# Performance work log

Measured on AMD Instinct MI355X. Metric: run time of the kernel, lower is better.

Reference implementation:

```python
import jax, jax.numpy as jnp
import numpy as np

NUM_CLASSES = 100000
FEAT_DIM = 128
BATCH = 16384
LOSS_WEIGHT = 0.01


def setup_inputs() -> dict:
    key = jax.random.key(0)
    k1, k2, k3 = jax.random.split(key, 3)
    y = jax.random.randint(k1, (BATCH,), 0, NUM_CLASSES, dtype=jnp.int64)
    feat = jax.random.normal(k2, (BATCH, FEAT_DIM), dtype=jnp.float32)
    centers = jax.random.normal(k3, (NUM_CLASSES, FEAT_DIM), dtype=jnp.float32)
    return {"y": y, "feat": feat, "centers": centers}


def reference(y, feat, centers):
    # hist: per-class counts (torch.histc with unit-width bins over [0, num_classes])
    counts = jax.ops.segment_sum(jnp.ones((feat.shape[0],), feat.dtype), y,
                                 num_segments=NUM_CLASSES)  # [C]
    # per-class mean of features; zeros for empty classes (sum is 0 there)
    feat_sum = jax.ops.segment_sum(feat, y, num_segments=NUM_CLASSES)  # [C, D]
    feat_mean = feat_sum / jnp.maximum(counts, 1.0)[:, None]
    ratio = counts / (1.0 + counts)  # hist / (1 + hist)
    centers_grad = ratio[:, None] * (centers - feat_mean)  # [C, D]
    diff = feat - centers[y]  # gather centers per sample
    loss = LOSS_WEIGHT * 0.5 * jnp.sum(diff * diff)
    return (loss, centers_grad)
```

## Files before the change

### kernel.cpp

```cpp
#include <hip/hip_runtime.h>


#define BATCH   16384
#define FEAT    128
#define NCLASS  100000
#define LOSS_W  0.01f
#define CAP     32
#define NPART   12500

typedef float v4f __attribute__((ext_vector_type(4)));

__global__ __launch_bounds__(256)
void k_hist(const int* __restrict__ y,
            int* __restrict__ cnt,
            int* __restrict__ bucket) {
    int i = blockIdx.x * 256 + threadIdx.x;
    int c = y[i];
    int r = atomicAdd(cnt + c, 1);
    if (r < CAP) bucket[c * CAP + r] = i;
}

__global__ __launch_bounds__(256)
void k_grad_loss(const float* __restrict__ centers,
                 const int* __restrict__ cnt,
                 const int* __restrict__ bucket,
                 const float* __restrict__ feat,
                 float* __restrict__ grad,
                 float* __restrict__ partial) {
    int wid  = (blockIdx.x * 256 + threadIdx.x) >> 6;
    int lane = threadIdx.x & 63;
    int c    = wid * 2 + (lane >> 5);
    int q    = lane & 31;
    int n = cnt[c];

    v4f ce = (v4f)(0.0f);
    if (n > 0)
        ce = __builtin_nontemporal_load(
                 (const v4f*)(centers + (size_t)c * FEAT) + q);

    int m = n < CAP ? n : CAP;
    v4f acc = (v4f)(0.0f);
    float ls = 0.0f;
    for (int k = 0; k < m; k++) {
        int i = bucket[c * CAP + k];
        v4f f = __builtin_nontemporal_load(
                    (const v4f*)(feat + (size_t)i * FEAT) + q);
        acc += f;
        v4f d = f - ce;
        ls += d.x*d.x + d.y*d.y + d.z*d.z + d.w*d.w;
    }

    v4f o = (v4f)(0.0f);
    if (n > 0) {
        float inv   = 1.0f / (float)n;
        float ratio = (float)n / (1.0f + (float)n);
        o = ratio * (ce - acc * inv);
    }
    __builtin_nontemporal_store(o, (v4f*)(grad + (size_t)c * FEAT) + q);

    #pragma unroll
    for (int off = 32; off > 0; off >>= 1)
        ls += __shfl_down(ls, off, 64);
    __shared__ float smem[4];
    if (lane == 0) smem[threadIdx.x >> 6] = ls;
    __syncthreads();
    if (threadIdx.x == 0)
        partial[blockIdx.x] = smem[0] + smem[1] + smem[2] + smem[3];
}

__global__ __launch_bounds__(256)
void k_loss_final(const float* __restrict__ partial,
                  float* __restrict__ loss) {
    float s = 0.0f;
    const v4f* p4 = (const v4f*)partial;
    for (int i = threadIdx.x; i < NPART / 4; i += 256) {
        v4f v = p4[i];
        s += v.x + v.y + v.z + v.w;
    }
    #pragma unroll
    for (int off = 32; off > 0; off >>= 1)
        s += __shfl_down(s, off, 64);
    __shared__ float smem[4];
    if ((threadIdx.x & 63) == 0) smem[threadIdx.x >> 6] = s;
    __syncthreads();
    if (threadIdx.x == 0)
        *loss = LOSS_W * 0.5f * (smem[0] + smem[1] + smem[2] + smem[3]);
}

extern "C" void kernel_launch(void* const* d_in, const int* in_sizes, int n_in,
                              void* d_out, int out_size, void* d_ws, size_t ws_size,
                              hipStream_t stream) {
    const int*   y       = (const int*)d_in[0];
    const float* feat    = (const float*)d_in[1];
    const float* centers = (const float*)d_in[2];

    float* loss = (float*)d_out;
    float* grad = (float*)d_out + 1;

    int*   cnt     = (int*)d_ws;
    int*   bucket  = cnt + NCLASS;
    float* partial = (float*)(bucket + (size_t)NCLASS * CAP);

    (void)hipMemsetAsync(cnt, 0, (size_t)NCLASS * sizeof(int), stream);

    k_hist<<<BATCH / 256, 256, 0, stream>>>(y, cnt, bucket);

    k_grad_loss<<<NPART, 256, 0, stream>>>(
        centers, cnt, bucket, feat, grad, partial);

    k_loss_final<<<1, 256, 0, stream>>>(partial, loss);
}
```

Before: 125.5 us.

## Move loss into histogram kernel and fold final reduction into grad launch

The squared-error loss is now computed per sample in the histogram kernel, which gathers centers by label, instead of per class inside the gradient kernel. The gradient kernel gets one extra block that reduces the 1024 partial sums into the loss, which removes the separate single-block final reduction launch. This cuts one kernel launch and the serial tail reduction over 12500 partials, and slims the gradient loop. In exchange, feat is read twice and centers gathered an extra time, adding memory traffic. The loss now also counts samples beyond the per-class bucket cap.

```diff
diff --git a/kernel.cpp b/kernel.cpp
--- a/kernel.cpp
+++ b/kernel.cpp
@@ -6,27 +6,71 @@
 #define NCLASS  100000
 #define LOSS_W  0.01f
 #define CAP     32
-#define NPART   12500
+#define NGRAD   12500
+#define K1_BLK  1024
 
 typedef float v4f __attribute__((ext_vector_type(4)));
 
 __global__ __launch_bounds__(256)
-void k_hist(const int* __restrict__ y,
-            int* __restrict__ cnt,
-            int* __restrict__ bucket) {
-    int i = blockIdx.x * 256 + threadIdx.x;
-    int c = y[i];
-    int r = atomicAdd(cnt + c, 1);
-    if (r < CAP) bucket[c * CAP + r] = i;
+void k_hist_loss(const int* __restrict__ y,
+                 const float* __restrict__ feat,
+                 const float* __restrict__ centers,
+                 int* __restrict__ cnt,
+                 int* __restrict__ bucket,
+                 float* __restrict__ partial) {
+    int tid = blockIdx.x * 256 + threadIdx.x;
+
+    if (tid < BATCH) {
+        int c = y[tid];
+        int r = atomicAdd(cnt + c, 1);
+        if (r < CAP) bucket[c * CAP + r] = tid;
+    }
+
+    int hw = tid >> 5;
+    int q  = tid & 31;
+    float ls = 0.0f;
+    #pragma unroll
+    for (int s = 0; s < 2; s++) {
+        int i = hw * 2 + s;
+        int c = y[i];
+        v4f f  = *((const v4f*)(feat    + (size_t)i * FEAT) + q);
+        v4f ce = *((const v4f*)(centers + (size_t)c * FEAT) + q);
+        v4f d = f - ce;
+        ls += d.x*d.x + d.y*d.y + d.z*d.z + d.w*d.w;
+    }
+
+    #pragma unroll
+    for (int off = 32; off > 0; off >>= 1)
+        ls += __shfl_down(ls, off, 64);
+    __shared__ float smem[4];
+    if ((threadIdx.x & 63) == 0) smem[threadIdx.x >> 6] = ls;
+    __syncthreads();
+    if (threadIdx.x == 0)
+        partial[blockIdx.x] = smem[0] + smem[1] + smem[2] + smem[3];
 }
 
 __global__ __launch_bounds__(256)
-void k_grad_loss(const float* __restrict__ centers,
-                 const int* __restrict__ cnt,
-                 const int* __restrict__ bucket,
-                 const float* __restrict__ feat,
-                 float* __restrict__ grad,
-                 float* __restrict__ partial) {
+void k_grad(const float* __restrict__ centers,
+            const int* __restrict__ cnt,
+            const int* __restrict__ bucket,
+            const float* __restrict__ feat,
+            float* __restrict__ grad,
+            const float* __restrict__ partial,
+            float* __restrict__ loss) {
+    if (blockIdx.x == NGRAD) {
+        v4f v = ((const v4f*)partial)[threadIdx.x];
+        float s = v.x + v.y + v.z + v.w;
+        #pragma unroll
+        for (int off = 32; off > 0; off >>= 1)
+            s += __shfl_down(s, off, 64);
+        __shared__ float sm[4];
+        if ((threadIdx.x & 63) == 0) sm[threadIdx.x >> 6] = s;
+        __syncthreads();
+        if (threadIdx.x == 0)
+            *loss = LOSS_W * 0.5f * (sm[0] + sm[1] + sm[2] + sm[3]);
+        return;
+    }
+
     int wid  = (blockIdx.x * 256 + threadIdx.x) >> 6;
     int lane = threadIdx.x & 63;
     int c    = wid * 2 + (lane >> 5);
@@ -40,14 +84,11 @@
 
     int m = n < CAP ? n : CAP;
     v4f acc = (v4f)(0.0f);
-    float ls = 0.0f;
     for (int k = 0; k < m; k++) {
         int i = bucket[c * CAP + k];
         v4f f = __builtin_nontemporal_load(
                     (const v4f*)(feat + (size_t)i * FEAT) + q);
         acc += f;
-        v4f d = f - ce;
-        ls += d.x*d.x + d.y*d.y + d.z*d.z + d.w*d.w;
     }
 
     v4f o = (v4f)(0.0f);
@@ -57,34 +98,6 @@
         o = ratio * (ce - acc * inv);
     }
     __builtin_nontemporal_store(o, (v4f*)(grad + (size_t)c * FEAT) + q);
-
-    #pragma unroll
-    for (int off = 32; off > 0; off >>= 1)
-        ls += __shfl_down(ls, off, 64);
-    __shared__ float smem[4];
-    if (lane == 0) smem[threadIdx.x >> 6] = ls;
-    __syncthreads();
-    if (threadIdx.x == 0)
-        partial[blockIdx.x] = smem[0] + smem[1] + smem[2] + smem[3];
-}
-
-__global__ __launch_bounds__(256)
-void k_loss_final(const float* __restrict__ partial,
-                  float* __restrict__ loss) {
-    float s = 0.0f;
-    const v4f* p4 = (const v4f*)partial;
-    for (int i = threadIdx.x; i < NPART / 4; i += 256) {
-        v4f v = p4[i];
-        s += v.x + v.y + v.z + v.w;
-    }
-    #pragma unroll
-    for (int off = 32; off > 0; off >>= 1)
-        s += __shfl_down(s, off, 64);
-    __shared__ float smem[4];
-    if ((threadIdx.x & 63) == 0) smem[threadIdx.x >> 6] = s;
-    __syncthreads();
-    if (threadIdx.x == 0)
-        *loss = LOSS_W * 0.5f * (smem[0] + smem[1] + smem[2] + smem[3]);
 }
 
 extern "C" void kernel_launch(void* const* d_in, const int* in_sizes, int n_in,
@@ -103,10 +116,8 @@
 
     (void)hipMemsetAsync(cnt, 0, (size_t)NCLASS * sizeof(int), stream);
 
-    k_hist<<<BATCH / 256, 256, 0, stream>>>(y, cnt, bucket);
+    k_hist_loss<<<K1_BLK, 256, 0, stream>>>(y, feat, centers, cnt, bucket, partial);
 
-    k_grad_loss<<<NPART, 256, 0, stream>>>(
-        centers, cnt, bucket, feat, grad, partial);
-
-    k_loss_final<<<1, 256, 0, stream>>>(partial, loss);
+    k_grad<<<NGRAD + 1, 256, 0, stream>>>(
+        centers, cnt, bucket, feat, grad, partial, loss);
 }
```

New measurement: 117.6 us. 1.07x faster.
